# Kernel optimization log

Hardware: AMD Instinct MI355X
Metric: run time of the kernel (lower is better)

## Reference

```python
import jax, jax.numpy as jnp
import numpy as np

B = 16
LEN_X = [1024, 896, 768, 640, 512, 1000, 750, 600, 1024, 512, 700, 800, 900, 950, 650, 550]
LEN_M = LEN_X[::-1]
MAXX, MAXM = 1024, 1024
D, H, DH, DFF = 512, 8, 64, 2048
EPS = 1e-5


def _ids(lens):
    seg = np.repeat(np.arange(len(lens)), lens).astype(np.int32)
    pos = np.concatenate([np.arange(l) for l in lens]).astype(np.int32)
    return seg, pos


def _layernorm(x, g, b):
    m = jnp.mean(x, axis=-1, keepdims=True)
    v = jnp.mean((x - m) ** 2, axis=-1, keepdims=True)  # biased var, as torch LN
    return (x - m) * jax.lax.rsqrt(v + EPS) * g + b


def setup_inputs() -> dict:
    key = jax.random.key(0)
    ks = jax.random.split(key, 8)
    TX, TM = sum(LEN_X), sum(LEN_M)
    seg_x, pos_x = _ids(LEN_X)
    seg_m, pos_m = _ids(LEN_M)

    def xavier(k, shape):  # nn.init.xavier_uniform_
        a = float(np.sqrt(6.0 / (shape[0] + shape[1])))
        return jax.random.uniform(k, shape, jnp.float32, -a, a)

    return {
        "x": jax.random.normal(ks[0], (TX, D), jnp.float32),
        "mem": jax.random.normal(ks[1], (TM, D), jnp.float32),
        "Wq": xavier(ks[2], (H * DH, D)),
        "Wk": xavier(ks[3], (H * DH, D)),
        "Wv": xavier(ks[4], (H * DH, D)),
        "Wo": xavier(ks[5], (D, H * DH)),
        "W1": xavier(ks[6], (DFF, D)),
        "b1": jnp.zeros((DFF,), jnp.float32),
        "W2": xavier(ks[7], (D, DFF)),
        "b2": jnp.zeros((D,), jnp.float32),
        "g_in": jnp.ones((D,), jnp.float32),
        "b_in": jnp.zeros((D,), jnp.float32),
        "g_inter": jnp.ones((D,), jnp.float32),
        "b_inter": jnp.zeros((D,), jnp.float32),
        "lengths_x": jnp.array(LEN_X, jnp.int32),
        "lengths_mem": jnp.array(LEN_M, jnp.int32),
        "seg_x": jnp.array(seg_x),
        "pos_x": jnp.array(pos_x),
        "seg_m": jnp.array(seg_m),
        "pos_m": jnp.array(pos_m),
    }


def reference(x, mem, Wq, Wk, Wv, Wo, W1, b1, W2, b2,
              g_in, b_in, g_inter, b_inter,
              lengths_x, lengths_mem, seg_x, pos_x, seg_m, pos_m):
    # --- self_attention(norm_in(x), mem) ---
    h = _layernorm(x, g_in, b_in)
    q = (h @ Wq.T).reshape(-1, H, DH)     # [Tx,H,DH]
    k = (mem @ Wk.T).reshape(-1, H, DH)   # [Tm,H,DH]
    v = (mem @ Wv.T).reshape(-1, H, DH)

    # pad_packed_tensor via scatter (value 0)
    qp = jnp.zeros((B, MAXX, H, DH), q.dtype).at[seg_x, pos_x].set(q)
    kp = jnp.zeros((B, MAXM, H, DH), k.dtype).at[seg_m, pos_m].set(k)
    vp = jnp.zeros((B, MAXM, H, DH), v.dtype).at[seg_m, pos_m].set(v)

    e = jnp.einsum('bxhd,byhd->bhxy', qp, kp) / np.sqrt(DH)  # [B,H,X,Y]

    xm = jnp.arange(MAXX)[None, :] < lengths_x[:, None]   # [B,X]
    ym = jnp.arange(MAXM)[None, :] < lengths_mem[:, None]  # [B,Y]
    mask = (xm[:, :, None] & ym[:, None, :])[:, None]      # [B,1,X,Y]

    e = jnp.where(mask, e, -1e9)
    alpha = jax.nn.softmax(e, axis=-1)
    alpha = jnp.where(mask, alpha, 0.0)

    out = jnp.einsum('bhxy,byhd->bxhd', alpha, vp)         # [B,X,H,DH]
    out = out.reshape(B, MAXX, H * DH) @ Wo.T              # [B,X,D]
    attn = out[seg_x, pos_x]                               # pack_padded_tensor

    x = x + attn
    # --- FFN block ---
    h2 = _layernorm(x, g_inter, b_inter)
    x = x + (jax.nn.relu(h2 @ W1.T + b1) @ W2.T + b2)
    return x
```

## Files before the change

### kernel.cpp

```cpp
#include <hip/hip_runtime.h>

#define TXT 12276
#define DM  512
#define NH  8
#define DHD 64
#define DFF 2048

typedef _Float16 half_t;
typedef _Float16 half8 __attribute__((ext_vector_type(8)));
typedef _Float16 half4v __attribute__((ext_vector_type(4)));
typedef float f32x4 __attribute__((ext_vector_type(4)));

__constant__ int c_offx[16] = {0,1024,1920,2688,3328,3840,4840,5590,6190,7214,7726,8426,9226,10126,11076,11726};
__constant__ int c_lenx[16] = {1024,896,768,640,512,1000,750,600,1024,512,700,800,900,950,650,550};
__constant__ int c_offm[16] = {0,550,1200,2150,3050,3850,4550,5062,6086,6686,7436,8436,8948,9588,10356,11252};
__constant__ int c_lenm[16] = {550,650,950,900,800,700,512,1024,600,750,1000,512,640,768,896,1024};
__constant__ int c_qtcum[17] = {0,16,30,42,52,60,76,88,98,114,122,133,146,161,176,187,196};

enum { EPI_NONE = 0, EPI_RES = 1, EPI_BIAS_RELU = 2, EPI_BIAS_RES = 3 };

__device__ __forceinline__ void gload_lds16(const void* g, void* l) {
    __builtin_amdgcn_global_load_lds((const __attribute__((address_space(1))) uint32_t*)g,
                                     (__attribute__((address_space(3))) uint32_t*)l, 16, 0, 0);
}

template<int EPI, int OUT_HALF, int PIPE>
__global__ __launch_bounds__(256)
void gemm_h(const half_t* __restrict__ A, const half_t* __restrict__ B,
            void* __restrict__ Cv, const float* __restrict__ bias,
            const float* __restrict__ res, int M, int N, int K)
{
    constexpr int NBUF = PIPE ? 2 : 1;
    __shared__ __align__(16) half_t As[NBUF*128*64];
    __shared__ __align__(16) half_t Bs[NBUF*128*64];

    const int t    = threadIdx.x;
    const int lane = t & 63;
    const int wv   = t >> 6;
    const int id   = blockIdx.x;
    const int wid  = (id & 7) * (gridDim.x >> 3) + (id >> 3);
    const int NY   = N >> 7;
    const int m0   = (wid / NY) * 128;
    const int n0   = (wid % NY) * 128;
    const int wr   = (wv >> 1) * 64;
    const int wc   = (wv & 1) * 64;
    const int fr   = lane & 15;
    const int fq   = lane >> 4;
    const int srow   = lane >> 3;
    const int schunk = (lane & 7) ^ srow;

    f32x4 acc[4][4];
    #pragma unroll
    for (int m = 0; m < 4; ++m)
        #pragma unroll
        for (int n = 0; n < 4; ++n) acc[m][n] = (f32x4){0.f,0.f,0.f,0.f};

    auto stage = [&](int k0, half_t* as, half_t* bs) {
        #pragma unroll
        for (int jj = 0; jj < 4; ++jj) {
            const int j    = wv * 4 + jj;
            const int rowt = j * 8 + srow;
            int ra = m0 + rowt; ra = (ra < M) ? ra : (M - 1);
            gload_lds16(A + (size_t)ra * K + k0 + schunk * 8, as + j * 512);
            gload_lds16(B + (size_t)(n0 + rowt) * K + k0 + schunk * 8, bs + j * 512);
        }
    };
    auto compute = [&](const half_t* as, const half_t* bs) {
        #pragma unroll
        for (int kk = 0; kk < 2; ++kk) {
            half8 af[4], bf[4];
            #pragma unroll
            for (int m = 0; m < 4; ++m) {
                const int row  = wr + m * 16 + fr;
                const int boff = (kk * 64 + fq * 16) ^ ((row & 7) << 4);
                af[m] = *(const half8*)((const char*)as + row * 128 + boff);
            }
            #pragma unroll
            for (int n = 0; n < 4; ++n) {
                const int row  = wc + n * 16 + fr;
                const int boff = (kk * 64 + fq * 16) ^ ((row & 7) << 4);
                bf[n] = *(const half8*)((const char*)bs + row * 128 + boff);
            }
            #pragma unroll
            for (int m = 0; m < 4; ++m)
                #pragma unroll
                for (int n = 0; n < 4; ++n)
                    acc[m][n] = __builtin_amdgcn_mfma_f32_16x16x32_f16(af[m], bf[n], acc[m][n], 0, 0, 0);
        }
    };

    if (PIPE == 0) {
        for (int k0 = 0; k0 < K; k0 += 64) {
            stage(k0, As, Bs);
            __syncthreads();
            compute(As, Bs);
            __syncthreads();
        }
    } else {
        stage(0, As, Bs);
        if (PIPE == 1) __syncthreads();
        int cur = 0;
        for (int k0 = 0; k0 < K; k0 += 64) {
            const bool nxt = (k0 + 64 < K);
            if (nxt)
                stage(k0 + 64, As + (cur ^ 1) * 8192, Bs + (cur ^ 1) * 8192);
            if (PIPE == 2) {
                if (nxt) asm volatile("s_waitcnt vmcnt(8)" ::: "memory");
                else     asm volatile("s_waitcnt vmcnt(0)" ::: "memory");
                __builtin_amdgcn_s_barrier();
                asm volatile("" ::: "memory");
            }
            compute(As + cur * 8192, Bs + cur * 8192);
            if (PIPE == 2) {
                if (nxt) {
                    asm volatile("" ::: "memory");
                    __builtin_amdgcn_s_barrier();
                }
            } else {
                __syncthreads();
            }
            cur ^= 1;
        }
    }

    #pragma unroll
    for (int n = 0; n < 4; ++n) {
        const int col = n0 + wc + n * 16 + fr;
        const float bsv = (EPI == EPI_BIAS_RELU || EPI == EPI_BIAS_RES) ? bias[col] : 0.f;
        #pragma unroll
        for (int m = 0; m < 4; ++m) {
            const f32x4 a = acc[m][n];
            #pragma unroll
            for (int r = 0; r < 4; ++r) {
                const int row = m0 + wr + m * 16 + fq * 4 + r;
                if (row < M) {
                    float v = a[r];
                    if (EPI == EPI_BIAS_RELU || EPI == EPI_BIAS_RES) v += bsv;
                    if (EPI == EPI_BIAS_RELU) v = fmaxf(v, 0.f);
                    if (EPI == EPI_RES || EPI == EPI_BIAS_RES) v += res[(size_t)row * N + col];
                    if (OUT_HALF) ((half_t*)Cv)[(size_t)row * N + col] = (half_t)v;
                    else          ((float*) Cv)[(size_t)row * N + col] = v;
                }
            }
        }
    }
}

__global__ __launch_bounds__(256)
void f2h_all(const float* __restrict__ Wq, const float* __restrict__ Wk,
             const float* __restrict__ Wv, const float* __restrict__ Wo,
             const float* __restrict__ W1, const float* __restrict__ W2,
             const float* __restrict__ mem,
             half_t* __restrict__ HW, half_t* __restrict__ H1)
{
    const int i = blockIdx.x * 256 + threadIdx.x;
    const float* src; int off; half_t* dst; int dbase;
    if      (i < 65536)   { src = Wq;  off = 0;       dst = HW; dbase = 0; }
    else if (i < 131072)  { src = Wk;  off = 65536;   dst = HW; dbase = 0; }
    else if (i < 196608)  { src = Wv;  off = 131072;  dst = HW; dbase = 0; }
    else if (i < 262144)  { src = Wo;  off = 196608;  dst = HW; dbase = 0; }
    else if (i < 524288)  { src = W1;  off = 262144;  dst = HW; dbase = 0; }
    else if (i < 786432)  { src = W2;  off = 524288;  dst = HW; dbase = 0; }
    else                  { src = mem; off = 786432;  dst = H1; dbase = 786432; }
    float4 v = ((const float4*)src)[i - off];
    half4v h = {(_Float16)v.x, (_Float16)v.y, (_Float16)v.z, (_Float16)v.w};
    ((half4v*)dst)[i - dbase] = h;
}

template<int OUT_HALF>
__global__ __launch_bounds__(256)
void layernorm_k(const float* __restrict__ in, const float* __restrict__ g,
                 const float* __restrict__ b, void* __restrict__ outv, int nrows)
{
    const int wave = threadIdx.x >> 6;
    const int lane = threadIdx.x & 63;
    const int row  = blockIdx.x * 4 + wave;
    if (row >= nrows) return;
    const float* px = in + (size_t)row * DM;
    float4 v0 = *(const float4*)(px + lane*4);
    float4 v1 = *(const float4*)(px + 256 + lane*4);

    float s = v0.x+v0.y+v0.z+v0.w + v1.x+v1.y+v1.z+v1.w;
    #pragma unroll
    for (int off = 1; off < 64; off <<= 1) s += __shfl_xor(s, off);
    float mean = s * (1.f/512.f);

    float dx0 = v0.x-mean, dy0 = v0.y-mean, dz0 = v0.z-mean, dw0 = v0.w-mean;
    float dx1 = v1.x-mean, dy1 = v1.y-mean, dz1 = v1.z-mean, dw1 = v1.w-mean;
    float q = dx0*dx0+dy0*dy0+dz0*dz0+dw0*dw0 + dx1*dx1+dy1*dy1+dz1*dz1+dw1*dw1;
    #pragma unroll
    for (int off = 1; off < 64; off <<= 1) q += __shfl_xor(q, off);
    float inv = rsqrtf(q * (1.f/512.f) + 1e-5f);

    float4 g0 = *(const float4*)(g + lane*4);
    float4 g1 = *(const float4*)(g + 256 + lane*4);
    float4 b0 = *(const float4*)(b + lane*4);
    float4 b1 = *(const float4*)(b + 256 + lane*4);
    float4 o0, o1;
    o0.x = dx0*inv*g0.x + b0.x; o0.y = dy0*inv*g0.y + b0.y;
    o0.z = dz0*inv*g0.z + b0.z; o0.w = dw0*inv*g0.w + b0.w;
    o1.x = dx1*inv*g1.x + b1.x; o1.y = dy1*inv*g1.y + b1.y;
    o1.z = dz1*inv*g1.z + b1.z; o1.w = dw1*inv*g1.w + b1.w;

    if (OUT_HALF) {
        half_t* po = (half_t*)outv + (size_t)row * DM;
        half4v h0 = {(_Float16)o0.x,(_Float16)o0.y,(_Float16)o0.z,(_Float16)o0.w};
        half4v h1 = {(_Float16)o1.x,(_Float16)o1.y,(_Float16)o1.z,(_Float16)o1.w};
        *(half4v*)(po + lane*4)       = h0;
        *(half4v*)(po + 256 + lane*4) = h1;
    } else {
        float* po = (float*)outv + (size_t)row * DM;
        *(float4*)(po + lane*4)       = o0;
        *(float4*)(po + 256 + lane*4) = o1;
    }
}

__global__ __launch_bounds__(256)
void attn_k(const half_t* __restrict__ q, const half_t* __restrict__ k,
            const half_t* __restrict__ v, half_t* __restrict__ o, int ldkv)
{
    __shared__ __align__(16) half_t Qs[64*64];
    __shared__ __align__(16) half_t Ks[2][64*64];
    __shared__ __align__(16) half_t Vt[2][64*64];
    __shared__ __align__(16) half_t Ps[4*16*72];

    const int t    = threadIdx.x;
    const int lane = t & 63;
    const int w    = t >> 6;
    const int fr   = lane & 15;
    const int fq   = lane >> 4;
    const int id   = blockIdx.x;
    const int hh   = id & 7;
    const int tile = id >> 3;
    int b = 0;
    while (tile >= c_qtcum[b+1]) ++b;
    const int qt0 = (tile - c_qtcum[b]) * 64;
    const int lx = c_lenx[b], lm = c_lenm[b];
    const int ox = c_offx[b], om = c_offm[b];
    const int qrem = lx - qt0;

    const int srow   = lane >> 3;
    const int schunk = (lane & 7) ^ srow;

    #pragma unroll
    for (int jj = 0; jj < 2; ++jj) {
        const int j   = w * 2 + jj;
        const int row = j * 8 + srow;
        const int rc  = (row < qrem) ? row : qrem - 1;
        gload_lds16(q + (size_t)(ox + qt0 + rc) * DM + hh * DHD + schunk * 8, &Qs[j * 512]);
    }

    const int nt = (lm + 63) >> 6;

    auto stageK = [&](int yt, int buf) {
        const int y0 = yt * 64, yrem = lm - y0;
        #pragma unroll
        for (int jj = 0; jj < 2; ++jj) {
            const int j   = w * 2 + jj;
            const int row = j * 8 + srow;
            const int rc  = (row < yrem) ? row : yrem - 1;
            gload_lds16(k + (size_t)(om + y0 + rc) * ldkv + hh * DHD + schunk * 8, &Ks[buf][j * 512]);
        }
    };
    auto loadV = [&](int yt, half8& va, half8& vb) {
        const int y0 = yt * 64, yrem = lm - y0;
        const int y  = lane;
        const int yc = (y < yrem) ? y : yrem - 1;
        const half_t* vp = v + (size_t)(om + y0 + yc) * ldkv + hh * DHD;
        va = *(const half8*)(vp + w * 8);
        vb = *(const half8*)(vp + (w + 4) * 8);
    };
    auto writeV = [&](int buf, half8 va, half8 vb) {
        const int y = lane;
        #pragma unroll
        for (int jd = 0; jd < 8; ++jd) {
            const int da = w * 8 + jd;
            const int db = (w + 4) * 8 + jd;
            *(half_t*)((char*)&Vt[buf][0] + da * 128 + ((2 * y) ^ ((da & 7) << 4))) = va[jd];
            *(half_t*)((char*)&Vt[buf][0] + db * 128 + ((2 * y) ^ ((db & 7) << 4))) = vb[jd];
        }
    };

    {
        stageK(0, 0);
        half8 va, vb;
        loadV(0, va, vb);
        writeV(0, va, vb);
    }
    __syncthreads();

    const int qrow = w * 16 + fr;
    const half8 q0 = *(const half8*)((const char*)Qs + qrow * 128 + ((0 * 64 + fq * 16) ^ ((qrow & 7) << 4)));
    const half8 q1 = *(const half8*)((const char*)Qs + qrow * 128 + ((1 * 64 + fq * 16) ^ ((qrow & 7) << 4)));

    f32x4 accO[4];
    float m_run = -1e30f, l_run = 0.f;
    #pragma unroll
    for (int n = 0; n < 4; ++n) accO[n] = (f32x4){0.f,0.f,0.f,0.f};

    int buf = 0;
    for (int yt = 0; yt < nt; ++yt) {
        const int yrem = lm - yt * 64;
        const bool pf = (yt + 1 < nt);
        half8 va, vb;
        if (pf) {
            stageK(yt + 1, buf ^ 1);
            loadV(yt + 1, va, vb);
        }

        const half_t* ks = &Ks[buf][0];
        const half_t* vt = &Vt[buf][0];

        f32x4 s[4];
        #pragma unroll
        for (int n = 0; n < 4; ++n) s[n] = (f32x4){0.f,0.f,0.f,0.f};
        #pragma unroll
        for (int kk = 0; kk < 2; ++kk) {
            const half8 aq = (kk == 0) ? q0 : q1;
            #pragma unroll
            for (int n = 0; n < 4; ++n) {
                const int krow = n * 16 + fr;
                half8 bk = *(const half8*)((const char*)ks + krow * 128 + ((kk * 64 + fq * 16) ^ ((krow & 7) << 4)));
                s[n] = __builtin_amdgcn_mfma_f32_16x16x32_f16(bk, aq, s[n], 0, 0, 0);
            }
        }

        #pragma unroll
        for (int n = 0; n < 4; ++n)
            #pragma unroll
            for (int r = 0; r < 4; ++r) {
                const int kv = n * 16 + fq * 4 + r;
                s[n][r] = (kv < yrem) ? s[n][r] * 0.125f : -1e9f;
            }

        float mx = s[0][0];
        #pragma unroll
        for (int n = 0; n < 4; ++n)
            #pragma unroll
            for (int r = 0; r < 4; ++r) mx = fmaxf(mx, s[n][r]);
        mx = fmaxf(mx, __shfl_xor(mx, 16));
        mx = fmaxf(mx, __shfl_xor(mx, 32));
        const float mnew = fmaxf(m_run, mx);
        const float sc   = __expf(m_run - mnew);
        m_run = mnew;
        float rs = 0.f;
        #pragma unroll
        for (int n = 0; n < 4; ++n)
            #pragma unroll
            for (int r = 0; r < 4; ++r) {
                const float pv = __expf(s[n][r] - mnew);
                s[n][r] = pv;
                rs += pv;
            }
        rs += __shfl_xor(rs, 16);
        rs += __shfl_xor(rs, 32);
        l_run = l_run * sc + rs;
        #pragma unroll
        for (int n = 0; n < 4; ++n)
            #pragma unroll
            for (int r = 0; r < 4; ++r) accO[n][r] *= sc;

        half_t* psw = &Ps[w * 1152];
        #pragma unroll
        for (int n = 0; n < 4; ++n)
            #pragma unroll
            for (int r = 0; r < 4; ++r)
                psw[fr * 72 + n * 16 + fq * 4 + r] = (half_t)s[n][r];

        #pragma unroll
        for (int kk = 0; kk < 2; ++kk) {
            half8 ap = *(const half8*)((const char*)psw + fr * 144 + fq * 16 + kk * 64);
            #pragma unroll
            for (int n = 0; n < 4; ++n) {
                const int d = n * 16 + fr;
                half8 bv = *(const half8*)((const char*)vt + d * 128 + ((kk * 64 + fq * 16) ^ ((d & 7) << 4)));
                accO[n] = __builtin_amdgcn_mfma_f32_16x16x32_f16(bv, ap, accO[n], 0, 0, 0);
            }
        }

        if (pf) writeV(buf ^ 1, va, vb);
        __syncthreads();
        buf ^= 1;
    }

    const int qq = w * 16 + fr;
    if (qq < qrem) {
        const float inv = 1.f / l_run;
        half_t* po = o + (size_t)(ox + qt0 + qq) * DM + hh * DHD;
        #pragma unroll
        for (int n = 0; n < 4; ++n) {
            half4v hv = {(_Float16)(accO[n][0] * inv), (_Float16)(accO[n][1] * inv),
                         (_Float16)(accO[n][2] * inv), (_Float16)(accO[n][3] * inv)};
            *(half4v*)(po + n * 16 + fq * 4) = hv;
        }
    }
}

extern "C" void kernel_launch(void* const* d_in, const int* in_sizes, int n_in,
                              void* d_out, int out_size, void* d_ws, size_t ws_size,
                              hipStream_t stream)
{
    (void)in_sizes; (void)n_in; (void)out_size; (void)ws_size;
    const float* x    = (const float*)d_in[0];
    const float* mem  = (const float*)d_in[1];
    const float* Wq   = (const float*)d_in[2];
    const float* Wk   = (const float*)d_in[3];
    const float* Wv   = (const float*)d_in[4];
    const float* Wo   = (const float*)d_in[5];
    const float* W1   = (const float*)d_in[6];
    const float* b1   = (const float*)d_in[7];
    const float* W2   = (const float*)d_in[8];
    const float* b2   = (const float*)d_in[9];
    const float* g_in = (const float*)d_in[10];
    const float* b_in = (const float*)d_in[11];
    const float* g_it = (const float*)d_in[12];
    const float* b_it = (const float*)d_in[13];
    float* out = (float*)d_out;
    float* ws  = (float*)d_ws;

    const size_t u = (size_t)TXT * DM;
    float*  F0  = ws;
    half_t* H0  = (half_t*)(ws + u);
    half_t* H1  = H0 + u;
    half_t* Hq  = H1 + u;
    half_t* Hkv = Hq + u;
    half_t* HW  = Hkv + 2*u;
    half_t* f1  = H1;

    half_t* hWq = HW;
    half_t* hWk = HW +  262144;
    half_t* hWo = HW +  786432;
    half_t* hW1 = HW + 1048576;
    half_t* hW2 = HW + 2097152;

    const dim3 blk(256);
    const int mt = (TXT + 127) / 128;

    f2h_all<<<dim3(9210), blk, 0, stream>>>(Wq, Wk, Wv, Wo, W1, W2, mem, HW, H1);

    layernorm_k<1><<<dim3(TXT/4), blk, 0, stream>>>(x, g_in, b_in, H0, TXT);

    gemm_h<EPI_NONE,1,2><<<dim3(mt*4), blk, 0, stream>>>(H0, hWq, Hq, nullptr, nullptr, TXT, 512, 512);
    gemm_h<EPI_NONE,1,0><<<dim3(mt*8), blk, 0, stream>>>(H1, hWk, Hkv, nullptr, nullptr, TXT, 1024, 512);

    attn_k<<<dim3(1568), blk, 0, stream>>>(Hq, Hkv, Hkv + 512, H1, 1024);

    gemm_h<EPI_RES,0,2><<<dim3(mt*4), blk, 0, stream>>>(H1, hWo, F0, nullptr, x, TXT, 512, 512);

    layernorm_k<1><<<dim3(TXT/4), blk, 0, stream>>>(F0, g_it, b_it, H0, TXT);

    gemm_h<EPI_BIAS_RELU,1,0><<<dim3(mt*16), blk, 0, stream>>>(H0, hW1, f1, b1, nullptr, TXT, 2048, 512);

    gemm_h<EPI_BIAS_RES,0,2><<<dim3(mt*4), blk, 0, stream>>>(f1, hW2, out, b2, F0, TXT, 512, 2048);
}
```

Baseline: 380.9 us.

## Add 128x64 GEMM tile for N=512 GEMMs and lazy softmax rescaling

After: 337.2 us. 1.13x faster.

```diff
diff --git a/kernel.cpp b/kernel.cpp
--- a/kernel.cpp
+++ b/kernel.cpp
@@ -98,27 +98,13 @@
         }
     } else {
         stage(0, As, Bs);
-        if (PIPE == 1) __syncthreads();
+        __syncthreads();
         int cur = 0;
         for (int k0 = 0; k0 < K; k0 += 64) {
-            const bool nxt = (k0 + 64 < K);
-            if (nxt)
+            if (k0 + 64 < K)
                 stage(k0 + 64, As + (cur ^ 1) * 8192, Bs + (cur ^ 1) * 8192);
-            if (PIPE == 2) {
-                if (nxt) asm volatile("s_waitcnt vmcnt(8)" ::: "memory");
-                else     asm volatile("s_waitcnt vmcnt(0)" ::: "memory");
-                __builtin_amdgcn_s_barrier();
-                asm volatile("" ::: "memory");
-            }
             compute(As + cur * 8192, Bs + cur * 8192);
-            if (PIPE == 2) {
-                if (nxt) {
-                    asm volatile("" ::: "memory");
-                    __builtin_amdgcn_s_barrier();
-                }
-            } else {
-                __syncthreads();
-            }
+            __syncthreads();
             cur ^= 1;
         }
     }
@@ -129,6 +115,108 @@
         const float bsv = (EPI == EPI_BIAS_RELU || EPI == EPI_BIAS_RES) ? bias[col] : 0.f;
         #pragma unroll
         for (int m = 0; m < 4; ++m) {
+            const f32x4 a = acc[m][n];
+            #pragma unroll
+            for (int r = 0; r < 4; ++r) {
+                const int row = m0 + wr + m * 16 + fq * 4 + r;
+                if (row < M) {
+                    float v = a[r];
+                    if (EPI == EPI_BIAS_RELU || EPI == EPI_BIAS_RES) v += bsv;
+                    if (EPI == EPI_BIAS_RELU) v = fmaxf(v, 0.f);
+                    if (EPI == EPI_RES || EPI == EPI_BIAS_RES) v += res[(size_t)row * N + col];
+                    if (OUT_HALF) ((half_t*)Cv)[(size_t)row * N + col] = (half_t)v;
+                    else          ((float*) Cv)[(size_t)row * N + col] = v;
+                }
+            }
+        }
+    }
+}
+
+template<int EPI, int OUT_HALF>
+__global__ __launch_bounds__(256)
+void gemm_h64(const half_t* __restrict__ A, const half_t* __restrict__ B,
+              void* __restrict__ Cv, const float* __restrict__ bias,
+              const float* __restrict__ res, int M, int N, int K)
+{
+    __shared__ __align__(16) half_t As[2*128*64];
+    __shared__ __align__(16) half_t Bs[2*64*64];
+
+    const int t    = threadIdx.x;
+    const int lane = t & 63;
+    const int wv   = t >> 6;
+    const int id   = blockIdx.x;
+    const int wid  = (id & 7) * (gridDim.x >> 3) + (id >> 3);
+    const int NY   = N >> 6;
+    const int m0   = (wid / NY) * 128;
+    const int n0   = (wid % NY) * 64;
+    const int wr   = wv * 32;
+    const int fr   = lane & 15;
+    const int fq   = lane >> 4;
+    const int srow   = lane >> 3;
+    const int schunk = (lane & 7) ^ srow;
+
+    f32x4 acc[2][4];
+    #pragma unroll
+    for (int m = 0; m < 2; ++m)
+        #pragma unroll
+        for (int n = 0; n < 4; ++n) acc[m][n] = (f32x4){0.f,0.f,0.f,0.f};
+
+    auto stage = [&](int k0, half_t* as, half_t* bs) {
+        #pragma unroll
+        for (int jj = 0; jj < 4; ++jj) {
+            const int j    = wv * 4 + jj;
+            const int rowt = j * 8 + srow;
+            int ra = m0 + rowt; ra = (ra < M) ? ra : (M - 1);
+            gload_lds16(A + (size_t)ra * K + k0 + schunk * 8, as + j * 512);
+        }
+        #pragma unroll
+        for (int jj = 0; jj < 2; ++jj) {
+            const int j    = wv * 2 + jj;
+            const int rowt = j * 8 + srow;
+            gload_lds16(B + (size_t)(n0 + rowt) * K + k0 + schunk * 8, bs + j * 512);
+        }
+    };
+    auto compute = [&](const half_t* as, const half_t* bs) {
+        #pragma unroll
+        for (int kk = 0; kk < 2; ++kk) {
+            half8 af[2], bf[4];
+            #pragma unroll
+            for (int m = 0; m < 2; ++m) {
+                const int row  = wr + m * 16 + fr;
+                const int boff = (kk * 64 + fq * 16) ^ ((row & 7) << 4);
+                af[m] = *(const half8*)((const char*)as + row * 128 + boff);
+            }
+            #pragma unroll
+            for (int n = 0; n < 4; ++n) {
+                const int row  = n * 16 + fr;
+                const int boff = (kk * 64 + fq * 16) ^ ((row & 7) << 4);
+                bf[n] = *(const half8*)((const char*)bs + row * 128 + boff);
+            }
+            #pragma unroll
+            for (int m = 0; m < 2; ++m)
+                #pragma unroll
+                for (int n = 0; n < 4; ++n)
+                    acc[m][n] = __builtin_amdgcn_mfma_f32_16x16x32_f16(af[m], bf[n], acc[m][n], 0, 0, 0);
+        }
+    };
+
+    stage(0, As, Bs);
+    __syncthreads();
+    int cur = 0;
+    for (int k0 = 0; k0 < K; k0 += 64) {
+        if (k0 + 64 < K)
+            stage(k0 + 64, As + (cur ^ 1) * 8192, Bs + (cur ^ 1) * 4096);
+        compute(As + cur * 8192, Bs + cur * 4096);
+        __syncthreads();
+        cur ^= 1;
+    }
+
+    #pragma unroll
+    for (int n = 0; n < 4; ++n) {
+        const int col = n0 + n * 16 + fr;
+        const float bsv = (EPI == EPI_BIAS_RELU || EPI == EPI_BIAS_RES) ? bias[col] : 0.f;
+        #pragma unroll
+        for (int m = 0; m < 2; ++m) {
             const f32x4 a = acc[m][n];
             #pragma unroll
             for (int r = 0; r < 4; ++r) {
@@ -325,13 +413,20 @@
             }
         }
 
-        #pragma unroll
-        for (int n = 0; n < 4; ++n)
-            #pragma unroll
-            for (int r = 0; r < 4; ++r) {
-                const int kv = n * 16 + fq * 4 + r;
-                s[n][r] = (kv < yrem) ? s[n][r] * 0.125f : -1e9f;
-            }
+        if (yrem >= 64) {
+            #pragma unroll
+            for (int n = 0; n < 4; ++n)
+                #pragma unroll
+                for (int r = 0; r < 4; ++r) s[n][r] *= 0.125f;
+        } else {
+            #pragma unroll
+            for (int n = 0; n < 4; ++n)
+                #pragma unroll
+                for (int r = 0; r < 4; ++r) {
+                    const int kv = n * 16 + fq * 4 + r;
+                    s[n][r] = (kv < yrem) ? s[n][r] * 0.125f : -1e9f;
+                }
+        }
 
         float mx = s[0][0];
         #pragma unroll
@@ -340,32 +435,36 @@
             for (int r = 0; r < 4; ++r) mx = fmaxf(mx, s[n][r]);
         mx = fmaxf(mx, __shfl_xor(mx, 16));
         mx = fmaxf(mx, __shfl_xor(mx, 32));
-        const float mnew = fmaxf(m_run, mx);
-        const float sc   = __expf(m_run - mnew);
-        m_run = mnew;
+        if (!__all(mx <= m_run + 8.f)) {
+            const float mnew = fmaxf(m_run, mx);
+            const float sc   = __expf(m_run - mnew);
+            m_run = mnew;
+            l_run *= sc;
+            #pragma unroll
+            for (int n = 0; n < 4; ++n)
+                #pragma unroll
+                for (int r = 0; r < 4; ++r) accO[n][r] *= sc;
+        }
         float rs = 0.f;
         #pragma unroll
         for (int n = 0; n < 4; ++n)
             #pragma unroll
             for (int r = 0; r < 4; ++r) {
-                const float pv = __expf(s[n][r] - mnew);
+                const float pv = __expf(s[n][r] - m_run);
                 s[n][r] = pv;
                 rs += pv;
             }
         rs += __shfl_xor(rs, 16);
         rs += __shfl_xor(rs, 32);
-        l_run = l_run * sc + rs;
-        #pragma unroll
-        for (int n = 0; n < 4; ++n)
-            #pragma unroll
-            for (int r = 0; r < 4; ++r) accO[n][r] *= sc;
+        l_run += rs;
 
         half_t* psw = &Ps[w * 1152];
         #pragma unroll
-        for (int n = 0; n < 4; ++n)
-            #pragma unroll
-            for (int r = 0; r < 4; ++r)
-                psw[fr * 72 + n * 16 + fq * 4 + r] = (half_t)s[n][r];
+        for (int n = 0; n < 4; ++n) {
+            half4v p4 = {(_Float16)s[n][0], (_Float16)s[n][1],
+                         (_Float16)s[n][2], (_Float16)s[n][3]};
+            *(half4v*)(psw + fr * 72 + n * 16 + fq * 4) = p4;
+        }
 
         #pragma unroll
         for (int kk = 0; kk < 2; ++kk) {
@@ -440,16 +539,16 @@
 
     layernorm_k<1><<<dim3(TXT/4), blk, 0, stream>>>(x, g_in, b_in, H0, TXT);
 
-    gemm_h<EPI_NONE,1,2><<<dim3(mt*4), blk, 0, stream>>>(H0, hWq, Hq, nullptr, nullptr, TXT, 512, 512);
+    gemm_h64<EPI_NONE,1><<<dim3(mt*8), blk, 0, stream>>>(H0, hWq, Hq, nullptr, nullptr, TXT, 512, 512);
     gemm_h<EPI_NONE,1,0><<<dim3(mt*8), blk, 0, stream>>>(H1, hWk, Hkv, nullptr, nullptr, TXT, 1024, 512);
 
     attn_k<<<dim3(1568), blk, 0, stream>>>(Hq, Hkv, Hkv + 512, H1, 1024);
 
-    gemm_h<EPI_RES,0,2><<<dim3(mt*4), blk, 0, stream>>>(H1, hWo, F0, nullptr, x, TXT, 512, 512);
+    gemm_h64<EPI_RES,0><<<dim3(mt*8), blk, 0, stream>>>(H1, hWo, F0, nullptr, x, TXT, 512, 512);
 
     layernorm_k<1><<<dim3(TXT/4), blk, 0, stream>>>(F0, g_it, b_it, H0, TXT);
 
     gemm_h<EPI_BIAS_RELU,1,0><<<dim3(mt*16), blk, 0, stream>>>(H0, hW1, f1, b1, nullptr, TXT, 2048, 512);
 
-    gemm_h<EPI_BIAS_RES,0,2><<<dim3(mt*4), blk, 0, stream>>>(f1, hW2, out, b2, F0, TXT, 512, 2048);
-}
+    gemm_h64<EPI_BIAS_RES,0><<<dim3(mt*8), blk, 0, stream>>>(f1, hW2, out, b2, F0, TXT, 512, 2048);
+}
```
